# Performance work log

Measured on AMD Instinct MI355X. Metric: run time of the kernel, lower is better.

Reference implementation:

```python
import jax, jax.numpy as jnp
import numpy as np

N = 100000   # nodes
E = 1600000  # edges
F_IN = 256   # input features
H = 128      # hidden
C = 40       # classes


def setup_inputs() -> dict:
    key = jax.random.key(0)
    ks = jax.random.split(key, 6)
    x = jax.random.normal(ks[0], (N, F_IN), dtype=jnp.float32)
    edge_index = jax.random.randint(ks[1], (2, E), 0, N, dtype=jnp.int32)
    edge_attr = jax.random.uniform(ks[2], (E,), dtype=jnp.float32)
    # Glorot-style init like GCNConv
    W1 = jax.random.normal(ks[3], (F_IN, H), dtype=jnp.float32) * (1.0 / np.sqrt(F_IN))
    b1 = jnp.zeros((H,), dtype=jnp.float32)
    W2 = jax.random.normal(ks[4], (H, C), dtype=jnp.float32) * (1.0 / np.sqrt(H))
    b2 = jnp.zeros((C,), dtype=jnp.float32)
    return {"x": x, "edge_index": edge_index, "edge_attr": edge_attr,
            "W1": W1, "b1": b1, "W2": W2, "b2": b2}


def _gcn_norm(edge_index, edge_weight, num_nodes):
    # PyG gcn_norm: add self-loops (weight 1), symmetric D^{-1/2} A D^{-1/2}
    row, col = edge_index[0], edge_index[1]
    loop = jnp.arange(num_nodes, dtype=row.dtype)
    row = jnp.concatenate([row, loop])
    col = jnp.concatenate([col, loop])
    ew = jnp.concatenate([edge_weight, jnp.ones((num_nodes,), edge_weight.dtype)])
    deg = jax.ops.segment_sum(ew, col, num_segments=num_nodes)
    dinv = jnp.where(deg > 0, jax.lax.rsqrt(deg), 0.0)
    norm = dinv[row] * ew * dinv[col]
    return row, col, norm


def _gcn_conv(x, row, col, norm, W, b):
    h = x @ W                              # [N, out] dense transform first
    msg = h[row] * norm[:, None]           # gather source + edge scaling
    out = jax.ops.segment_sum(msg, col, num_segments=x.shape[0])  # scatter-add
    return out + b


def reference(x, edge_index, edge_attr, W1, b1, W2, b2):
    row, col, norm = _gcn_norm(edge_index, edge_attr, x.shape[0])
    h = _gcn_conv(x, row, col, norm, W1, b1)
    h = jax.nn.relu(h)
    # dropout is identity in eval mode
    h = _gcn_conv(h, row, col, norm, W2, b2)
    return jax.nn.log_softmax(h, axis=1)
```

## Files before the change

### kernel.cpp

```cpp
#include <hip/hip_runtime.h>

#define N_NODES 100000
#define N_EDGES 1600000
#define F_INPUT 256
#define H_DIM   128
#define C_DIM   40
#define NBKT    391
#define NCHK    1563
#define NGEMM1  1563
#define NPREB   152

typedef short  bf8   __attribute__((ext_vector_type(8)));
typedef float  f32x4 __attribute__((ext_vector_type(4)));
typedef float  f32x2 __attribute__((ext_vector_type(2)));
typedef unsigned short u16x8 __attribute__((ext_vector_type(8)));

static __device__ __forceinline__ unsigned short f2bf(float f) {
    union { float f; unsigned u; } v; v.f = f;
    unsigned r = v.u + 0x7FFFu + ((v.u >> 16) & 1u);
    return (unsigned short)(r >> 16);
}
static __device__ __forceinline__ f32x2 bfpair(unsigned u) {
    union { unsigned u; float f; } lo, hi;
    lo.u = u << 16; hi.u = u & 0xFFFF0000u;
    return (f32x2){lo.f, hi.f};
}

__global__ void k_preh(const float* __restrict__ W1, const float* __restrict__ W2,
                       unsigned short* Wp1, unsigned short* Wp2,
                       const int* __restrict__ col, unsigned* __restrict__ histG) {
    int tid = threadIdx.x;
    if (blockIdx.x >= NPREB) {
        __shared__ unsigned histL[NBKT];
        int chunk = blockIdx.x - NPREB;
        for (int i = tid; i < NBKT; i += 256) histL[i] = 0;
        __syncthreads();
        int e0 = chunk * 1024 + tid;
#pragma unroll
        for (int k = 0; k < 4; k++) {
            int e = e0 + k * 256;
            if (e < N_EDGES) atomicAdd(&histL[col[e] >> 8], 1u);
        }
        __syncthreads();
        for (int i = tid; i < NBKT; i += 256) histG[(size_t)i * NCHK + chunk] = histL[i];
        return;
    }
    int idx = blockIdx.x * 256 + tid;
    if (idx < 32768) {
        int j = idx & 7, lane = (idx >> 3) & 63, ks = (idx >> 9) & 7, nt = idx >> 12;
        int m = lane & 15, q = lane >> 4;
        Wp1[idx] = f2bf(W1[(ks * 32 + q * 8 + j) * H_DIM + nt * 16 + m]);
    }
    int idx2 = idx - 32768;
    if (idx2 >= 0 && idx2 < 6144) {
        int j = idx2 & 7, lane = (idx2 >> 3) & 63, ks = (idx2 >> 9) & 3, nt = idx2 >> 11;
        int m = lane & 15, q = lane >> 4;
        int n = nt * 16 + m;
        Wp2[idx2] = (n < C_DIM) ? f2bf(W2[(ks * 32 + q * 8 + j) * C_DIM + n]) : (unsigned short)0;
    }
}

__global__ void k_scanB(unsigned* histG, unsigned* bktTotal) {
    __shared__ unsigned s[256];
    int B = blockIdx.x, t = threadIdx.x;
    unsigned carry = 0;
    for (int c0 = 0; c0 < NCHK; c0 += 256) {
        int idx = c0 + t;
        unsigned v = (idx < NCHK) ? histG[(size_t)B * NCHK + idx] : 0;
        s[t] = v; __syncthreads();
        for (int off = 1; off < 256; off <<= 1) {
            unsigned u = (t >= off) ? s[t - off] : 0;
            __syncthreads();
            s[t] += u;
            __syncthreads();
        }
        if (idx < NCHK) histG[(size_t)B * NCHK + idx] = s[t] - v + carry;
        unsigned tot = s[255];
        __syncthreads();
        carry += tot;
    }
    if (t == 0) bktTotal[B] = carry;
}

__global__ void k_scat1(const int* __restrict__ row, const int* __restrict__ col,
                        const float* __restrict__ ea,
                        const unsigned* __restrict__ histG,
                        const unsigned* __restrict__ bktTotal,
                        unsigned* __restrict__ bucketBase,
                        int2* __restrict__ recs) {
    __shared__ unsigned base_l[NBKT];
    __shared__ unsigned cursor[NBKT];
    __shared__ unsigned s[256];
    int blk = blockIdx.x, t = threadIdx.x;
    unsigned carry = 0;
    for (int c0 = 0; c0 < NBKT; c0 += 256) {
        int idx = c0 + t;
        unsigned v = (idx < NBKT) ? bktTotal[idx] : 0;
        s[t] = v; __syncthreads();
        for (int off = 1; off < 256; off <<= 1) {
            unsigned u = (t >= off) ? s[t - off] : 0;
            __syncthreads();
            s[t] += u;
            __syncthreads();
        }
        if (idx < NBKT) base_l[idx] = s[t] - v + carry;
        unsigned tot = s[255];
        __syncthreads();
        carry += tot;
    }
    __syncthreads();
    if (blk == 0) {
        for (int i = t; i < NBKT; i += 256) bucketBase[i] = base_l[i];
        if (t == 0) bucketBase[NBKT] = carry;
    }
    for (int i = t; i < NBKT; i += 256) {
        base_l[i] += histG[(size_t)i * NCHK + blk];
        cursor[i] = 0;
    }
    __syncthreads();
    int e0 = blk * 1024 + t;
#pragma unroll
    for (int k = 0; k < 4; k++) {
        int e = e0 + k * 256;
        if (e < N_EDGES) {
            int c = col[e];
            int bkt = c >> 8;
            unsigned r = atomicAdd(&cursor[bkt], 1u);
            int pos = (int)(base_l[bkt] + r);
            recs[pos] = make_int2((row[e] << 8) | (c & 255), __float_as_int(ea[e]));
        }
    }
}

__global__ void k_pass2(const int2* __restrict__ recs,
                        const unsigned* __restrict__ bucketBase,
                        int* __restrict__ start, int* __restrict__ cnt,
                        float* __restrict__ dinv, int2* __restrict__ csr) {
    __shared__ unsigned cntL[256];
    __shared__ unsigned wsL[256];
    __shared__ unsigned s[256];
    __shared__ int startL[256];
    __shared__ unsigned cur[256];
    int B = blockIdx.x, t = threadIdx.x;
    cntL[t] = 0; wsL[t] = 0; cur[t] = 0;
    __syncthreads();
    int lo = (int)bucketBase[B], hi = (int)bucketBase[B + 1];
    for (int i = lo + t; i < hi; i += 256) {
        int2 rc = recs[i];
        int cl = rc.x & 255;
        atomicAdd(&cntL[cl], 1u);
        unsigned q = __float2uint_rn(__int_as_float(rc.y) * 65536.0f);
        atomicAdd(&wsL[cl], q);
    }
    __syncthreads();
    unsigned v = cntL[t];
    s[t] = v; __syncthreads();
    for (int off = 1; off < 256; off <<= 1) {
        unsigned u = (t >= off) ? s[t - off] : 0;
        __syncthreads();
        s[t] += u;
        __syncthreads();
    }
    int st = lo + (int)(s[t] - v);
    startL[t] = st;
    int node = B * 256 + t;
    if (node < N_NODES) {
        start[node] = st;
        cnt[node] = (int)v;
        dinv[node] = rsqrtf((float)(65536u + wsL[t]) * (1.0f / 65536.0f));
    }
    __syncthreads();
    for (int i = lo + t; i < hi; i += 256) {
        int2 rc = recs[i];
        int cl = rc.x & 255;
        int rw = rc.x >> 8;
        unsigned r = atomicAdd(&cur[cl], 1u);
        csr[startL[cl] + (int)r] = make_int2(rw, rc.y);
    }
}

__global__ __launch_bounds__(256, 2) void k_gemm1(
        const float* __restrict__ x, const unsigned short* __restrict__ Wp,
        const float* __restrict__ dinv, unsigned short* __restrict__ h) {
    __shared__ unsigned short sWp[32768];
    __shared__ unsigned short lds_out[64 * H_DIM];
    int tid = threadIdx.x;
    int wave = tid >> 6, lane = tid & 63;
    int m = lane & 15, q = lane >> 4;
    int tile = blockIdx.x;
    int row0 = tile * 64 + wave * 16;
    int rowA = row0 + m; if (rowA >= N_NODES) rowA = N_NODES - 1;
    const float* xr = x + (long)rowA * F_INPUT + q * 8;

    float4 xv[16];
#pragma unroll
    for (int ks = 0; ks < 8; ks++) {
        xv[2 * ks]     = *(const float4*)(xr + ks * 32);
        xv[2 * ks + 1] = *(const float4*)(xr + ks * 32 + 4);
    }
#pragma unroll
    for (int it = 0; it < 16; it++) {
        int idx = (it * 256 + tid) * 8;
        *(u16x8*)(sWp + idx) = *(const u16x8*)(Wp + idx);
    }
    __syncthreads();

    f32x4 acc[8];
#pragma unroll
    for (int i = 0; i < 8; i++) acc[i] = (f32x4){0.f, 0.f, 0.f, 0.f};
#pragma unroll
    for (int ks = 0; ks < 8; ks++) {
        float4 a0 = xv[2 * ks], a1 = xv[2 * ks + 1];
        bf8 a;
        a[0] = (short)f2bf(a0.x); a[1] = (short)f2bf(a0.y);
        a[2] = (short)f2bf(a0.z); a[3] = (short)f2bf(a0.w);
        a[4] = (short)f2bf(a1.x); a[5] = (short)f2bf(a1.y);
        a[6] = (short)f2bf(a1.z); a[7] = (short)f2bf(a1.w);
#pragma unroll
        for (int nt = 0; nt < 8; nt++) {
            bf8 bb = *(const bf8*)(sWp + (((nt * 8 + ks) * 64 + lane) << 3));
            acc[nt] = __builtin_amdgcn_mfma_f32_16x16x32_bf16(a, bb, acc[nt], 0, 0, 0);
        }
    }
    int lrow = wave * 16 + q * 4;
    float dv[4];
#pragma unroll
    for (int r = 0; r < 4; r++) {
        int gr = tile * 64 + lrow + r; if (gr >= N_NODES) gr = N_NODES - 1;
        dv[r] = dinv[gr];
    }
#pragma unroll
    for (int nt = 0; nt < 8; nt++)
#pragma unroll
        for (int r = 0; r < 4; r++)
            lds_out[(lrow + r) * H_DIM + nt * 16 + m] = f2bf(acc[nt][r] * dv[r]);
    __syncthreads();
    int valid = N_NODES - tile * 64; if (valid > 64) valid = 64;
    unsigned short* gbase = h + (size_t)tile * 64 * H_DIM;
#pragma unroll
    for (int i = 0; i < 4; i++) {
        int idx = (i * 256 + tid) * 8;
        if (idx < valid * H_DIM)
            *(u16x8*)(gbase + idx) = *(const u16x8*)(lds_out + idx);
    }
}

__global__ __launch_bounds__(256) void k_agg1(
        const unsigned* __restrict__ hw, const int2* __restrict__ csr,
        const int* __restrict__ start, const int* __restrict__ cnt,
        const float* __restrict__ dinv, const float* __restrict__ b1,
        unsigned* __restrict__ h1w) {
    int c = blockIdx.x * 4 + (threadIdx.x >> 6);
    int lane = threadIdx.x & 63;
    if (c >= N_NODES) return;
    float di = dinv[c];
    int su = __builtin_amdgcn_readfirstlane(start[c]);
    int n  = __builtin_amdgcn_readfirstlane(cnt[c]);
    f32x2 acc = bfpair(hw[(size_t)c * 64 + lane]);
    int i = 0;
    for (; i + 4 <= n; i += 4) {
        int2 p0 = csr[su + i], p1 = csr[su + i + 1];
        int2 p2 = csr[su + i + 2], p3 = csr[su + i + 3];
        int r0 = __builtin_amdgcn_readfirstlane(p0.x);
        int r1 = __builtin_amdgcn_readfirstlane(p1.x);
        int r2 = __builtin_amdgcn_readfirstlane(p2.x);
        int r3 = __builtin_amdgcn_readfirstlane(p3.x);
        float w0 = __int_as_float(__builtin_amdgcn_readfirstlane(p0.y));
        float w1 = __int_as_float(__builtin_amdgcn_readfirstlane(p1.y));
        float w2 = __int_as_float(__builtin_amdgcn_readfirstlane(p2.y));
        float w3 = __int_as_float(__builtin_amdgcn_readfirstlane(p3.y));
        unsigned a0 = hw[(size_t)r0 * 64 + lane];
        unsigned a1 = hw[(size_t)r1 * 64 + lane];
        unsigned a2 = hw[(size_t)r2 * 64 + lane];
        unsigned a3 = hw[(size_t)r3 * 64 + lane];
        acc += (f32x2){w0, w0} * bfpair(a0);
        acc += (f32x2){w1, w1} * bfpair(a1);
        acc += (f32x2){w2, w2} * bfpair(a2);
        acc += (f32x2){w3, w3} * bfpair(a3);
    }
    for (; i < n; i++) {
        int2 p = csr[su + i];
        int r = __builtin_amdgcn_readfirstlane(p.x);
        float w = __int_as_float(__builtin_amdgcn_readfirstlane(p.y));
        unsigned a = hw[(size_t)r * 64 + lane];
        acc += (f32x2){w, w} * bfpair(a);
    }
    float2 bb = ((const float2*)b1)[lane];
    float o0 = fmaxf(di * acc.x + bb.x, 0.f);
    float o1 = fmaxf(di * acc.y + bb.y, 0.f);
    h1w[(size_t)c * 64 + lane] = (unsigned)f2bf(o0) | ((unsigned)f2bf(o1) << 16);
}

__global__ __launch_bounds__(256, 4) void k_gemm2(const unsigned short* __restrict__ h1,
                        const unsigned short* __restrict__ Wp,
                        const float* __restrict__ dinv,
                        unsigned short* __restrict__ h2) {
    __shared__ unsigned short lds_out[64 * C_DIM];
    int tid = threadIdx.x;
    int wave = tid >> 6, lane = tid & 63;
    int m = lane & 15, q = lane >> 4;
    int row0 = blockIdx.x * 64 + wave * 16;
    int rowA = row0 + m; if (rowA >= N_NODES) rowA = N_NODES - 1;

    f32x4 acc[3];
#pragma unroll
    for (int i = 0; i < 3; i++) acc[i] = (f32x4){0.f, 0.f, 0.f, 0.f};
    const unsigned short* hr = h1 + (long)rowA * H_DIM + q * 8;
#pragma unroll
    for (int ks = 0; ks < 4; ks++) {
        bf8 a = *(const bf8*)(hr + ks * 32);
#pragma unroll
        for (int nt = 0; nt < 3; nt++) {
            bf8 b = *(const bf8*)(Wp + (((nt * 4 + ks) * 64 + lane) << 3));
            acc[nt] = __builtin_amdgcn_mfma_f32_16x16x32_bf16(a, b, acc[nt], 0, 0, 0);
        }
    }
    int lrow = wave * 16 + q * 4;
    float dv[4];
#pragma unroll
    for (int r = 0; r < 4; r++) {
        int gr = blockIdx.x * 64 + lrow + r; if (gr >= N_NODES) gr = N_NODES - 1;
        dv[r] = dinv[gr];
    }
#pragma unroll
    for (int nt = 0; nt < 3; nt++)
#pragma unroll
        for (int r = 0; r < 4; r++) {
            int colo = nt * 16 + m;
            if (colo < C_DIM)
                lds_out[(lrow + r) * C_DIM + colo] = f2bf(acc[nt][r] * dv[r]);
        }
    __syncthreads();
    int valid = N_NODES - blockIdx.x * 64; if (valid > 64) valid = 64;
    unsigned short* gbase = h2 + (size_t)blockIdx.x * 64 * C_DIM;
    int total = valid * C_DIM;
#pragma unroll
    for (int i = 0; i < 3; i++) {
        int idx = (i * 256 + tid) * 4;
        if (idx < total)
            *(uint2*)(gbase + idx) = *(const uint2*)(lds_out + idx);
    }
}

__global__ void k_agg2(const unsigned short* __restrict__ h2, const int2* __restrict__ csr,
                       const int* __restrict__ start, const int* __restrict__ cnt,
                       const float* __restrict__ dinv, const float* __restrict__ b2,
                       float* __restrict__ out) {
    int c = (blockIdx.x * blockDim.x + threadIdx.x) >> 6;
    int lane = threadIdx.x & 63;
    if (c >= N_NODES) return;
    int eg = lane >> 3, cl = lane & 7;
    float di = dinv[c];
    int s = start[c];
    int n = cnt[c];

    float w[3]; int r[3];
#pragma unroll
    for (int t = 0; t < 3; t++) {
        int i = eg + 8 * t;
        int2 p = csr[s + ((i < n) ? i : 0)];
        bool val = (i < n);
        r[t] = val ? p.x : c;
        w[t] = val ? __int_as_float(p.y) : 0.f;
    }
    uint4 gv[3] = {{0,0,0,0},{0,0,0,0},{0,0,0,0}};
    uint4 selfv = {0, 0, 0, 0};
    if (cl < 5) {
#pragma unroll
        for (int t = 0; t < 3; t++)
            gv[t] = *(const uint4*)(h2 + (long)r[t] * C_DIM + cl * 8);
        if (eg == 0) selfv = *(const uint4*)(h2 + (long)c * C_DIM + cl * 8);
    }
    f32x2 acc[4];
#pragma unroll
    for (int k = 0; k < 4; k++) acc[k] = (f32x2){0.f, 0.f};
    {
        unsigned sv[4] = {selfv.x, selfv.y, selfv.z, selfv.w};
        if (eg == 0 && cl < 5)
#pragma unroll
            for (int k = 0; k < 4; k++) acc[k] += bfpair(sv[k]);
    }
#pragma unroll
    for (int t = 0; t < 3; t++) {
        unsigned vv[4] = {gv[t].x, gv[t].y, gv[t].z, gv[t].w};
        f32x2 ww = (f32x2){w[t], w[t]};
#pragma unroll
        for (int k = 0; k < 4; k++) acc[k] += ww * bfpair(vv[k]);
    }
    for (int i = 24 + eg; i < n; i += 8) {
        int2 p = csr[s + i];
        if (cl < 5) {
            uint4 v4 = *(const uint4*)(h2 + (long)p.x * C_DIM + cl * 8);
            unsigned vv[4] = {v4.x, v4.y, v4.z, v4.w};
            float wt = __int_as_float(p.y);
            f32x2 ww = (f32x2){wt, wt};
#pragma unroll
            for (int k = 0; k < 4; k++) acc[k] += ww * bfpair(vv[k]);
        }
    }
#pragma unroll
    for (int k = 0; k < 4; k++) {
        acc[k].x += __shfl_xor(acc[k].x, 8);  acc[k].y += __shfl_xor(acc[k].y, 8);
        acc[k].x += __shfl_xor(acc[k].x, 16); acc[k].y += __shfl_xor(acc[k].y, 16);
        acc[k].x += __shfl_xor(acc[k].x, 32); acc[k].y += __shfl_xor(acc[k].y, 32);
    }
    float v[8];
    float lm = -INFINITY;
    if (cl < 5) {
#pragma unroll
        for (int k = 0; k < 4; k++) {
            v[2 * k]     = di * acc[k].x + b2[cl * 8 + 2 * k];
            v[2 * k + 1] = di * acc[k].y + b2[cl * 8 + 2 * k + 1];
            lm = fmaxf(lm, fmaxf(v[2 * k], v[2 * k + 1]));
        }
    }
    lm = fmaxf(lm, __shfl_xor(lm, 1));
    lm = fmaxf(lm, __shfl_xor(lm, 2));
    lm = fmaxf(lm, __shfl_xor(lm, 4));
    float ls = 0.f;
    if (cl < 5) {
#pragma unroll
        for (int j = 0; j < 8; j++) ls += __expf(v[j] - lm);
    }
    ls += __shfl_xor(ls, 1);
    ls += __shfl_xor(ls, 2);
    ls += __shfl_xor(ls, 4);
    if (eg == 0 && cl < 5) {
        float lsm = lm + logf(ls);
        f32x4 o0, o1;
#pragma unroll
        for (int j = 0; j < 4; j++) { o0[j] = v[j] - lsm; o1[j] = v[j + 4] - lsm; }
        *(f32x4*)(out + (long)c * C_DIM + cl * 8)     = o0;
        *(f32x4*)(out + (long)c * C_DIM + cl * 8 + 4) = o1;
    }
}

extern "C" void kernel_launch(void* const* d_in, const int* in_sizes, int n_in,
                              void* d_out, int out_size, void* d_ws, size_t ws_size,
                              hipStream_t stream) {
    const float* x  = (const float*)d_in[0];
    const int*   ei = (const int*)d_in[1];
    const float* ea = (const float*)d_in[2];
    const float* W1 = (const float*)d_in[3];
    const float* b1 = (const float*)d_in[4];
    const float* W2 = (const float*)d_in[5];
    const float* b2 = (const float*)d_in[6];
    const int* row = ei;
    const int* col = ei + N_EDGES;

    char* ws = (char*)d_ws;
    size_t off = 0;
    auto alloc = [&](size_t bytes) -> void* {
        void* p = ws + off;
        off = (off + bytes + 255) & ~(size_t)255;
        return p;
    };
    unsigned*       histG   = (unsigned*)alloc((size_t)NBKT * NCHK * 4);
    unsigned*       bktTot  = (unsigned*)alloc((size_t)NBKT * 4);
    unsigned*       bktBase = (unsigned*)alloc((size_t)(NBKT + 1) * 4);
    int*            start   = (int*)alloc((size_t)N_NODES * 4);
    int*            cnt     = (int*)alloc((size_t)N_NODES * 4);
    float*          dinv    = (float*)alloc((size_t)N_NODES * 4);
    int2*           recs    = (int2*)alloc((size_t)N_EDGES * 8);
    int2*           csr     = (int2*)alloc((size_t)(N_EDGES + 8) * 8);
    unsigned short* Wp1     = (unsigned short*)alloc(32768 * 2);
    unsigned short* Wp2     = (unsigned short*)alloc(6144 * 2);
    unsigned short* h       = (unsigned short*)alloc((size_t)(N_NODES + 64) * H_DIM * 2);
    unsigned short* h1      = (unsigned short*)alloc((size_t)N_NODES * H_DIM * 2);
    unsigned short* h2      = (unsigned short*)alloc((size_t)(N_NODES + 64) * C_DIM * 2);

    k_preh<<<NPREB + NCHK, 256, 0, stream>>>(W1, W2, Wp1, Wp2, col, histG);
    k_scanB<<<NBKT, 256, 0, stream>>>(histG, bktTot);
    k_scat1<<<NCHK, 256, 0, stream>>>(row, col, ea, histG, bktTot, bktBase, recs);
    k_pass2<<<NBKT, 256, 0, stream>>>(recs, bktBase, start, cnt, dinv, csr);
    k_gemm1<<<NGEMM1, 256, 0, stream>>>(x, Wp1, dinv, h);
    k_agg1<<<N_NODES / 4, 256, 0, stream>>>((const unsigned*)h, csr, start, cnt, dinv, b1,
                                            (unsigned*)h1);
    k_gemm2<<<(N_NODES + 63) / 64, 256, 0, stream>>>(h1, Wp2, dinv, h2);
    k_agg2<<<N_NODES / 4, 256, 0, stream>>>(h2, csr, start, cnt, dinv, b2, (float*)d_out);
}
```

Baseline: 366.3 us.

## Hoist bucket scan, coarsen edge scatter blocks, and pad h2 rows to 64

The bucket-base prefix scan moves into its own single-block kernel, so the scatter blocks no longer each repeat it. The scatter kernel now runs 391 blocks of 512 threads. Each block covers four histogram chunks and takes its base from the first chunk's prefix. The bucket-pass kernel also moves to 512 threads, with guards on its 256-wide shared arrays. The layer-2 hidden buffer h2 is padded from 40 to 64 bf16 per row, so the aggregation gathers read from aligned rows, at the cost of a larger buffer and a strided write-out.

```diff
diff --git a/kernel.cpp b/kernel.cpp
--- a/kernel.cpp
+++ b/kernel.cpp
@@ -7,6 +7,7 @@
 #define C_DIM   40
 #define NBKT    391
 #define NCHK    1563
+#define NSC1    391
 #define NGEMM1  1563
 #define NPREB   152
 
@@ -82,16 +83,9 @@
     if (t == 0) bktTotal[B] = carry;
 }
 
-__global__ void k_scat1(const int* __restrict__ row, const int* __restrict__ col,
-                        const float* __restrict__ ea,
-                        const unsigned* __restrict__ histG,
-                        const unsigned* __restrict__ bktTotal,
-                        unsigned* __restrict__ bucketBase,
-                        int2* __restrict__ recs) {
-    __shared__ unsigned base_l[NBKT];
-    __shared__ unsigned cursor[NBKT];
+__global__ void k_scanC(const unsigned* __restrict__ bktTotal, unsigned* bucketBase) {
     __shared__ unsigned s[256];
-    int blk = blockIdx.x, t = threadIdx.x;
+    int t = threadIdx.x;
     unsigned carry = 0;
     for (int c0 = 0; c0 < NBKT; c0 += 256) {
         int idx = c0 + t;
@@ -103,25 +97,31 @@
             s[t] += u;
             __syncthreads();
         }
-        if (idx < NBKT) base_l[idx] = s[t] - v + carry;
+        if (idx < NBKT) bucketBase[idx] = s[t] - v + carry;
         unsigned tot = s[255];
         __syncthreads();
         carry += tot;
     }
-    __syncthreads();
-    if (blk == 0) {
-        for (int i = t; i < NBKT; i += 256) bucketBase[i] = base_l[i];
-        if (t == 0) bucketBase[NBKT] = carry;
-    }
-    for (int i = t; i < NBKT; i += 256) {
-        base_l[i] += histG[(size_t)i * NCHK + blk];
+    if (t == 0) bucketBase[NBKT] = carry;
+}
+
+__global__ void k_scat1(const int* __restrict__ row, const int* __restrict__ col,
+                        const float* __restrict__ ea,
+                        const unsigned* __restrict__ histG,
+                        const unsigned* __restrict__ bucketBase,
+                        int2* __restrict__ recs) {
+    __shared__ unsigned base_l[NBKT];
+    __shared__ unsigned cursor[NBKT];
+    int blk = blockIdx.x, t = threadIdx.x;
+    for (int i = t; i < NBKT; i += 512) {
+        base_l[i] = bucketBase[i] + histG[(size_t)i * NCHK + blk * 4];
         cursor[i] = 0;
     }
     __syncthreads();
-    int e0 = blk * 1024 + t;
-#pragma unroll
-    for (int k = 0; k < 4; k++) {
-        int e = e0 + k * 256;
+    int e0 = blk * 4096 + t;
+#pragma unroll
+    for (int k = 0; k < 8; k++) {
+        int e = e0 + k * 512;
         if (e < N_EDGES) {
             int c = col[e];
             int bkt = c >> 8;
@@ -142,10 +142,10 @@
     __shared__ int startL[256];
     __shared__ unsigned cur[256];
     int B = blockIdx.x, t = threadIdx.x;
-    cntL[t] = 0; wsL[t] = 0; cur[t] = 0;
+    if (t < 256) { cntL[t] = 0; wsL[t] = 0; cur[t] = 0; }
     __syncthreads();
     int lo = (int)bucketBase[B], hi = (int)bucketBase[B + 1];
-    for (int i = lo + t; i < hi; i += 256) {
+    for (int i = lo + t; i < hi; i += 512) {
         int2 rc = recs[i];
         int cl = rc.x & 255;
         atomicAdd(&cntL[cl], 1u);
@@ -153,24 +153,28 @@
         atomicAdd(&wsL[cl], q);
     }
     __syncthreads();
-    unsigned v = cntL[t];
-    s[t] = v; __syncthreads();
+    unsigned v = 0;
+    if (t < 256) { v = cntL[t]; s[t] = v; }
+    __syncthreads();
     for (int off = 1; off < 256; off <<= 1) {
-        unsigned u = (t >= off) ? s[t - off] : 0;
-        __syncthreads();
-        s[t] += u;
-        __syncthreads();
-    }
-    int st = lo + (int)(s[t] - v);
-    startL[t] = st;
-    int node = B * 256 + t;
-    if (node < N_NODES) {
-        start[node] = st;
-        cnt[node] = (int)v;
-        dinv[node] = rsqrtf((float)(65536u + wsL[t]) * (1.0f / 65536.0f));
-    }
-    __syncthreads();
-    for (int i = lo + t; i < hi; i += 256) {
+        unsigned u = 0;
+        if (t < 256 && t >= (unsigned)off) u = s[t - off];
+        __syncthreads();
+        if (t < 256) s[t] += u;
+        __syncthreads();
+    }
+    if (t < 256) {
+        int st = lo + (int)(s[t] - v);
+        startL[t] = st;
+        int node = B * 256 + t;
+        if (node < N_NODES) {
+            start[node] = st;
+            cnt[node] = (int)v;
+            dinv[node] = rsqrtf((float)(65536u + wsL[t]) * (1.0f / 65536.0f));
+        }
+    }
+    __syncthreads();
+    for (int i = lo + t; i < hi; i += 512) {
         int2 rc = recs[i];
         int cl = rc.x & 255;
         int rw = rc.x >> 8;
@@ -332,13 +336,11 @@
         }
     __syncthreads();
     int valid = N_NODES - blockIdx.x * 64; if (valid > 64) valid = 64;
-    unsigned short* gbase = h2 + (size_t)blockIdx.x * 64 * C_DIM;
-    int total = valid * C_DIM;
-#pragma unroll
-    for (int i = 0; i < 3; i++) {
-        int idx = (i * 256 + tid) * 4;
-        if (idx < total)
-            *(uint2*)(gbase + idx) = *(const uint2*)(lds_out + idx);
+    unsigned short* gbase = h2 + (size_t)blockIdx.x * 64 * 64;
+    int total10 = valid * 10;
+    for (int i = tid; i < total10; i += 256) {
+        int rw = i / 10, part = i - rw * 10;
+        *(uint2*)(gbase + rw * 64 + part * 4) = *(const uint2*)(lds_out + rw * C_DIM + part * 4);
     }
 }
 
@@ -368,8 +370,8 @@
     if (cl < 5) {
 #pragma unroll
         for (int t = 0; t < 3; t++)
-            gv[t] = *(const uint4*)(h2 + (long)r[t] * C_DIM + cl * 8);
-        if (eg == 0) selfv = *(const uint4*)(h2 + (long)c * C_DIM + cl * 8);
+            gv[t] = *(const uint4*)(h2 + (long)r[t] * 64 + cl * 8);
+        if (eg == 0) selfv = *(const uint4*)(h2 + (long)c * 64 + cl * 8);
     }
     f32x2 acc[4];
 #pragma unroll
@@ -390,7 +392,7 @@
     for (int i = 24 + eg; i < n; i += 8) {
         int2 p = csr[s + i];
         if (cl < 5) {
-            uint4 v4 = *(const uint4*)(h2 + (long)p.x * C_DIM + cl * 8);
+            uint4 v4 = *(const uint4*)(h2 + (long)p.x * 64 + cl * 8);
             unsigned vv[4] = {v4.x, v4.y, v4.z, v4.w};
             float wt = __int_as_float(p.y);
             f32x2 ww = (f32x2){wt, wt};
@@ -467,12 +469,13 @@
     unsigned short* Wp2     = (unsigned short*)alloc(6144 * 2);
     unsigned short* h       = (unsigned short*)alloc((size_t)(N_NODES + 64) * H_DIM * 2);
     unsigned short* h1      = (unsigned short*)alloc((size_t)N_NODES * H_DIM * 2);
-    unsigned short* h2      = (unsigned short*)alloc((size_t)(N_NODES + 64) * C_DIM * 2);
+    unsigned short* h2      = (unsigned short*)alloc((size_t)(N_NODES + 64) * 64 * 2);
 
     k_preh<<<NPREB + NCHK, 256, 0, stream>>>(W1, W2, Wp1, Wp2, col, histG);
     k_scanB<<<NBKT, 256, 0, stream>>>(histG, bktTot);
-    k_scat1<<<NCHK, 256, 0, stream>>>(row, col, ea, histG, bktTot, bktBase, recs);
-    k_pass2<<<NBKT, 256, 0, stream>>>(recs, bktBase, start, cnt, dinv, csr);
+    k_scanC<<<1, 256, 0, stream>>>(bktTot, bktBase);
+    k_scat1<<<NSC1, 512, 0, stream>>>(row, col, ea, histG, bktBase, recs);
+    k_pass2<<<NBKT, 512, 0, stream>>>(recs, bktBase, start, cnt, dinv, csr);
     k_gemm1<<<NGEMM1, 256, 0, stream>>>(x, Wp1, dinv, h);
     k_agg1<<<N_NODES / 4, 256, 0, stream>>>((const unsigned*)h, csr, start, cnt, dinv, b1,
                                             (unsigned*)h1);
```

New measurement: 362.5 us, median of 2. No clear change (-1.0%).
